# Kernel tuning notes

Hardware: AMD Instinct MI355X
Metric: run time of the kernel (lower is better)

Reference implementation:

```python
import jax, jax.numpy as jnp
import numpy as np

B, N, D = 8, 2048, 1024


def setup_inputs() -> dict:
    key = jax.random.key(0)
    k1, k2, k3, k4 = jax.random.split(key, 4)
    x = jax.random.normal(k1, (B, N, D), dtype=jnp.float32)
    f = jax.random.normal(k2, (B, N, D), dtype=jnp.float32)
    # nn.Linear(D, 1, bias=False) weights, shape [1, D]
    lim = 1.0 / np.sqrt(D)
    wk = jax.random.uniform(k3, (1, D), dtype=jnp.float32, minval=-lim, maxval=lim)
    wq = jax.random.uniform(k4, (1, D), dtype=jnp.float32, minval=-lim, maxval=lim)
    return {"x": x, "f": f, "wk": wk, "wq": wq}


def reference(x, f, wk, wq):
    # scalar k/q projections: [B, N]
    k = jnp.einsum("bnd,d->bn", x, wk[0])
    q = jnp.einsum("bnd,d->bn", x, wq[0])
    scale = 1.0 / jnp.sqrt(jnp.float32(D))
    # rank-1 outer-product scores: e[b,i,j] = k[b,i]*q[b,j]/sqrt(D)
    e = k[:, :, None] * q[:, None, :] * scale  # [B, N, N]
    # keep upper triangle (incl. diag), then any exact zero -> -inf
    # (faithful to torch: e_post[e_post == 0] = -inf, which also hits
    #  naturally-zero upper-triangle entries)
    e_tri = jnp.triu(e)
    e_post = jnp.where(e_tri == 0, -jnp.inf, e_tri)
    a = jax.nn.softmax(e_post, axis=1)  # softmax over rows (dim=1)
    # f_out = a^T @ f
    f_out = jnp.einsum("bij,bid->bjd", a, f)
    return f_out
```

## Files before the change

### kernel.cpp

```cpp
#include <hip/hip_runtime.h>

#define B 8
#define N 2048
#define D 1024
#define C 64
#define LC (N / C)
#define M 6
#define PB 96

__global__ __launch_bounds__(256) void k_proj(const float* __restrict__ x,
                                              const float* __restrict__ wk,
                                              const float* __restrict__ wq,
                                              float* __restrict__ kq) {
    const int wave = threadIdx.x >> 6;
    const int lane = threadIdx.x & 63;
    const int row  = blockIdx.x * 4 + wave;
    const float4* xr  = (const float4*)(x + (size_t)row * D);
    const float4* wk4 = (const float4*)wk;
    const float4* wq4 = (const float4*)wq;
    float ak = 0.f, aq = 0.f;
#pragma unroll
    for (int t = 0; t < (D / 4) / 64; ++t) {
        float4 xv = xr[t * 64 + lane];
        float4 kv = wk4[t * 64 + lane];
        float4 qv = wq4[t * 64 + lane];
        ak += xv.x * kv.x + xv.y * kv.y + xv.z * kv.z + xv.w * kv.w;
        aq += xv.x * qv.x + xv.y * qv.y + xv.z * qv.z + xv.w * qv.w;
    }
#pragma unroll
    for (int off = 32; off > 0; off >>= 1) {
        ak += __shfl_down(ak, off, 64);
        aq += __shfl_down(aq, off, 64);
    }
    if (lane == 0) {
        kq[row] = ak;
        kq[B * N + row] = aq;
    }
}

__global__ __launch_bounds__(128) void k_partial(const float* __restrict__ kq,
                                                 const float* __restrict__ f,
                                                 float* __restrict__ part) {
    const int dhalf = blockIdx.x & 1;
    const int c     = (blockIdx.x >> 1) & (C - 1);
    const int b     = blockIdx.x >> 7;
    const int d     = dhalf * 512 + threadIdx.x * 4;
    const float*  kb = kq + b * N + c * LC;
    const float4* fb = (const float4*)(f + (size_t)(b * N + c * LC) * D + d);
    float4 s[M];
#pragma unroll
    for (int m = 0; m < M; ++m) s[m] = make_float4(0.f, 0.f, 0.f, 0.f);
#pragma unroll 8
    for (int i = 0; i < LC; ++i) {
        float4 ff = fb[i * (D / 4)];
        float  kk = kb[i];
        float  w  = (kk != 0.0f) ? 1.0f : 0.0f;
        s[0].x += w * ff.x; s[0].y += w * ff.y; s[0].z += w * ff.z; s[0].w += w * ff.w;
        float kp = kk;
#pragma unroll
        for (int m = 1; m < M; ++m) {
            s[m].x += kp * ff.x; s[m].y += kp * ff.y;
            s[m].z += kp * ff.z; s[m].w += kp * ff.w;
            kp *= kk;
        }
    }
    float4* pb = (float4*)(part + ((size_t)(b * C + c) * M) * D + d);
#pragma unroll
    for (int m = 0; m < M; ++m) pb[m * (D / 4)] = s[m];
}

__global__ __launch_bounds__(128) void k_scan(const float* __restrict__ kq,
                                              float* __restrict__ Tc,
                                              float* __restrict__ part) {
    if (blockIdx.x < PB) {
        const int gid = blockIdx.x * 128 + threadIdx.x;
        const int d4  = gid & (D / 4 - 1);
        const int m   = (gid >> 8) % M;
        const int b   = gid / (256 * M);
        float4* p4 = (float4*)part;
        const size_t base = ((size_t)b * C * M + m) * (D / 4) + d4;
        const size_t cs   = (size_t)M * (D / 4);
        float4 run = make_float4(0.f, 0.f, 0.f, 0.f);
#pragma unroll 1
        for (int c0 = 0; c0 < C; c0 += 8) {
            float4 buf[8];
#pragma unroll
            for (int j = 0; j < 8; ++j) buf[j] = p4[base + (size_t)(c0 + j) * cs];
#pragma unroll
            for (int j = 0; j < 8; ++j) {
                float4 v = buf[j];
                p4[base + (size_t)(c0 + j) * cs] = run;
                run.x += v.x; run.y += v.y; run.z += v.z; run.w += v.w;
            }
        }
    } else {
        const int b2   = blockIdx.x - PB;
        const int lane = threadIdx.x;
        if (lane < 64) {
            float tm[M] = {0.f, 0.f, 0.f, 0.f, 0.f, 0.f};
            const float* kb = kq + b2 * N + lane * LC;
#pragma unroll
            for (int i = 0; i < LC; ++i) {
                float kk = kb[i];
                tm[0] += (kk != 0.0f) ? 1.0f : 0.0f;
                float kp = kk;
#pragma unroll
                for (int m = 1; m < M; ++m) { tm[m] += kp; kp *= kk; }
            }
#pragma unroll
            for (int m = 0; m < M; ++m) {
                float v = tm[m];
                const float orig = v;
#pragma unroll
                for (int off = 1; off < 64; off <<= 1) {
                    float nv = __shfl_up(v, off, 64);
                    if (lane >= off) v += nv;
                }
                Tc[(b2 * C + lane) * M + m] = v - orig;
            }
        }
    }
}

__global__ __launch_bounds__(128) void k_out(const float* __restrict__ kq,
                                             const float* __restrict__ f,
                                             const float* __restrict__ Tc,
                                             const float* __restrict__ part,
                                             float* __restrict__ out) {
    const int dhalf = blockIdx.x & 1;
    const int c     = (blockIdx.x >> 1) & (C - 1);
    const int b     = blockIdx.x >> 7;
    const int d     = dhalf * 512 + threadIdx.x * 4;

    float4 s[M];
    float  t[M];
    const float4* pb = (const float4*)(part + ((size_t)(b * C + c) * M) * D + d);
#pragma unroll
    for (int m = 0; m < M; ++m) s[m] = pb[m * (D / 4)];
#pragma unroll
    for (int m = 0; m < M; ++m) t[m] = Tc[(b * C + c) * M + m];

    const float*  kb = kq + b * N + c * LC;
    const float*  qb = kq + B * N + b * N + c * LC;
    const float4* fb = (const float4*)(f + (size_t)(b * N + c * LC) * D + d);
    float4*       ob = (float4*)(out + (size_t)(b * N + c * LC) * D + d);

#pragma unroll 4
    for (int i = 0; i < LC; ++i) {
        float4 ff = fb[i * (D / 4)];
        float  kk = kb[i];
        float  qq = qb[i];
        float  w  = (kk != 0.0f) ? 1.0f : 0.0f;
        t[0] += w;
        s[0].x += w * ff.x; s[0].y += w * ff.y; s[0].z += w * ff.z; s[0].w += w * ff.w;
        float kp = kk;
#pragma unroll
        for (int m = 1; m < M; ++m) {
            t[m] += kp;
            s[m].x += kp * ff.x; s[m].y += kp * ff.y;
            s[m].z += kp * ff.z; s[m].w += kp * ff.w;
            kp *= kk;
        }
        const float cj = qq * 0.03125f;
        const float g2 = cj * 0.5f;
        const float g3 = cj * (1.0f / 3.0f);
        const float g4 = cj * 0.25f;
        const float g5 = cj * 0.2f;
        float Z = ((((t[5] * g5 + t[4]) * g4 + t[3]) * g3 + t[2]) * g2 + t[1]) * cj + t[0];
        float rz = __builtin_amdgcn_rcpf(Z);
        float4 o;
        o.x = (((((s[5].x * g5 + s[4].x) * g4 + s[3].x) * g3 + s[2].x) * g2 + s[1].x) * cj + s[0].x) * rz;
        o.y = (((((s[5].y * g5 + s[4].y) * g4 + s[3].y) * g3 + s[2].y) * g2 + s[1].y) * cj + s[0].y) * rz;
        o.z = (((((s[5].z * g5 + s[4].z) * g4 + s[3].z) * g3 + s[2].z) * g2 + s[1].z) * cj + s[0].z) * rz;
        o.w = (((((s[5].w * g5 + s[4].w) * g4 + s[3].w) * g3 + s[2].w) * g2 + s[1].w) * cj + s[0].w) * rz;
        ob[i * (D / 4)] = o;
    }
}

extern "C" void kernel_launch(void* const* d_in, const int* in_sizes, int n_in,
                              void* d_out, int out_size, void* d_ws, size_t ws_size,
                              hipStream_t stream) {
    (void)in_sizes; (void)n_in; (void)out_size; (void)ws_size;
    const float* x  = (const float*)d_in[0];
    const float* f  = (const float*)d_in[1];
    const float* wk = (const float*)d_in[2];
    const float* wq = (const float*)d_in[3];
    float* out = (float*)d_out;
    float* ws  = (float*)d_ws;

    float* kq   = ws;
    float* Tc   = ws + 2 * B * N;
    float* part = ws + 2 * B * N + 4096;

    hipLaunchKernelGGL(k_proj,    dim3(B * N / 4),   dim3(256), 0, stream, x, wk, wq, kq);
    hipLaunchKernelGGL(k_partial, dim3(B * C * 2),   dim3(128), 0, stream, kq, f, part);
    hipLaunchKernelGGL(k_scan,    dim3(PB + B),      dim3(128), 0, stream, kq, Tc, part);
    hipLaunchKernelGGL(k_out,     dim3(B * C * 2),   dim3(128), 0, stream, kq, f, Tc, part, out);
}
```

Measured before the change: 195.8 us.

## Fuse four stages into one cooperative kernel with register-cached f

Replaces the four separate launches with a single cooperative kernel that uses grid-wide syncs between the projection, partial-sum, scan and output phases. Each thread keeps its 32 f values in registers between the partial and output phases, so f is read from memory once instead of twice, and the k/q slices are staged in shared memory. The cost is three grid barriers, heavy register use (64 floats of f per thread), and reliance on the occupancy check for co-residency. If cooperative launch is unavailable, the code falls back to the old four-kernel path.

Result: no change. 196.0 us (+0.1%).

```diff
diff --git a/kernel.cpp b/kernel.cpp
--- a/kernel.cpp
+++ b/kernel.cpp
@@ -1,4 +1,7 @@
 #include <hip/hip_runtime.h>
+#include <hip/hip_cooperative_groups.h>
+
+namespace cg = cooperative_groups;
 
 #define B 8
 #define N 2048
@@ -7,6 +10,175 @@
 #define LC (N / C)
 #define M 6
 #define PB 96
+#define GRID 1024
+#define TPB 256
+
+__global__ __launch_bounds__(TPB, 4) void k_fused(
+    const float* __restrict__ x, const float* __restrict__ f,
+    const float* __restrict__ wk, const float* __restrict__ wq,
+    float* __restrict__ kq, float* __restrict__ Tc,
+    float* __restrict__ part, float* __restrict__ out)
+{
+    cg::grid_group grid = cg::this_grid();
+    const int tid  = threadIdx.x;
+    const int blk  = blockIdx.x;
+    const int lane = tid & 63;
+
+    __shared__ float sk[LC];
+    __shared__ float sq[LC];
+
+    {
+        const int wave = (blk << 2) | (tid >> 6);
+        const float4* wk4 = (const float4*)wk;
+        const float4* wq4 = (const float4*)wq;
+        float4 kw[4], qw[4];
+#pragma unroll
+        for (int t = 0; t < 4; ++t) { kw[t] = wk4[t * 64 + lane]; qw[t] = wq4[t * 64 + lane]; }
+#pragma unroll
+        for (int r = 0; r < 4; ++r) {
+            const int row = (wave << 2) | r;
+            const float4* xr = (const float4*)(x + (size_t)row * D);
+            float ak = 0.f, aq = 0.f;
+#pragma unroll
+            for (int t = 0; t < 4; ++t) {
+                float4 xv = xr[t * 64 + lane];
+                ak += xv.x * kw[t].x + xv.y * kw[t].y + xv.z * kw[t].z + xv.w * kw[t].w;
+                aq += xv.x * qw[t].x + xv.y * qw[t].y + xv.z * qw[t].z + xv.w * qw[t].w;
+            }
+#pragma unroll
+            for (int off = 32; off > 0; off >>= 1) {
+                ak += __shfl_down(ak, off, 64);
+                aq += __shfl_down(aq, off, 64);
+            }
+            if (lane == 0) { kq[row] = ak; kq[B * N + row] = aq; }
+        }
+    }
+    __threadfence();
+    grid.sync();
+
+    const int dhalf = blk & 1;
+    const int c     = (blk >> 1) & (C - 1);
+    const int b     = blk >> 7;
+    const int d     = dhalf * 512 + tid * 2;
+
+    if (tid < LC)                        sk[tid]      = kq[b * N + c * LC + tid];
+    else if (tid >= 64 && tid < 64 + LC) sq[tid - 64] = kq[B * N + b * N + c * LC + (tid - 64)];
+    __syncthreads();
+
+    const float2* fb = (const float2*)(f + (size_t)(b * N + c * LC) * D + d);
+    float2 freg[LC];
+    float2 s[M];
+#pragma unroll
+    for (int m = 0; m < M; ++m) s[m] = make_float2(0.f, 0.f);
+#pragma unroll
+    for (int i = 0; i < LC; ++i) {
+        float2 ff = fb[i * (D / 2)];
+        freg[i] = ff;
+        float kk = sk[i];
+        float w  = (kk != 0.0f) ? 1.0f : 0.0f;
+        s[0].x += w * ff.x; s[0].y += w * ff.y;
+        float kp = kk;
+#pragma unroll
+        for (int m = 1; m < M; ++m) {
+            s[m].x += kp * ff.x; s[m].y += kp * ff.y;
+            kp *= kk;
+        }
+    }
+    {
+        float2* pw = (float2*)(part + ((size_t)(b * C + c) * M) * D + d);
+#pragma unroll
+        for (int m = 0; m < M; ++m) pw[m * (D / 2)] = s[m];
+    }
+    __threadfence();
+    grid.sync();
+
+    if (blk < PB) {
+        const int gid = blk * TPB + tid;
+        const int d2  = gid & (D / 2 - 1);
+        const int m   = (gid >> 9) % M;
+        const int bb  = (gid >> 9) / M;
+        float2* p2 = (float2*)part;
+        const size_t base = ((size_t)bb * C * M + m) * (D / 2) + d2;
+        const size_t cs   = (size_t)M * (D / 2);
+        float2 run = make_float2(0.f, 0.f);
+#pragma unroll 1
+        for (int c0 = 0; c0 < C; c0 += 8) {
+            float2 buf[8];
+#pragma unroll
+            for (int j = 0; j < 8; ++j) buf[j] = p2[base + (size_t)(c0 + j) * cs];
+#pragma unroll
+            for (int j = 0; j < 8; ++j) {
+                float2 v = buf[j];
+                p2[base + (size_t)(c0 + j) * cs] = run;
+                run.x += v.x; run.y += v.y;
+            }
+        }
+    } else if (blk < PB + 2) {
+        const int b2 = ((blk - PB) << 2) | (tid >> 6);
+        float tm[M] = {0.f, 0.f, 0.f, 0.f, 0.f, 0.f};
+        const float* kb = kq + b2 * N + lane * LC;
+#pragma unroll
+        for (int i = 0; i < LC; ++i) {
+            float kk = kb[i];
+            tm[0] += (kk != 0.0f) ? 1.0f : 0.0f;
+            float kp = kk;
+#pragma unroll
+            for (int m = 1; m < M; ++m) { tm[m] += kp; kp *= kk; }
+        }
+#pragma unroll
+        for (int m = 0; m < M; ++m) {
+            float v = tm[m];
+            const float orig = v;
+#pragma unroll
+            for (int off = 1; off < 64; off <<= 1) {
+                float nv = __shfl_up(v, off, 64);
+                if (lane >= off) v += nv;
+            }
+            Tc[(b2 * C + lane) * M + m] = v - orig;
+        }
+    }
+    __threadfence();
+    grid.sync();
+
+    {
+        float2 s2[M];
+        const float2* pr = (const float2*)(part + ((size_t)(b * C + c) * M) * D + d);
+#pragma unroll
+        for (int m = 0; m < M; ++m) s2[m] = pr[m * (D / 2)];
+        float t[M];
+#pragma unroll
+        for (int m = 0; m < M; ++m) t[m] = Tc[(b * C + c) * M + m];
+
+        float2* ob = (float2*)(out + (size_t)(b * N + c * LC) * D + d);
+#pragma unroll
+        for (int i = 0; i < LC; ++i) {
+            float2 ff = freg[i];
+            float kk = sk[i];
+            float qq = sq[i];
+            float w  = (kk != 0.0f) ? 1.0f : 0.0f;
+            t[0] += w;
+            s2[0].x += w * ff.x; s2[0].y += w * ff.y;
+            float kp = kk;
+#pragma unroll
+            for (int m = 1; m < M; ++m) {
+                t[m] += kp;
+                s2[m].x += kp * ff.x; s2[m].y += kp * ff.y;
+                kp *= kk;
+            }
+            const float cj = qq * 0.03125f;
+            const float g2 = cj * 0.5f;
+            const float g3 = cj * (1.0f / 3.0f);
+            const float g4 = cj * 0.25f;
+            const float g5 = cj * 0.2f;
+            float Z = ((((t[5] * g5 + t[4]) * g4 + t[3]) * g3 + t[2]) * g2 + t[1]) * cj + t[0];
+            float rz = __builtin_amdgcn_rcpf(Z);
+            float2 o;
+            o.x = (((((s2[5].x * g5 + s2[4].x) * g4 + s2[3].x) * g3 + s2[2].x) * g2 + s2[1].x) * cj + s2[0].x) * rz;
+            o.y = (((((s2[5].y * g5 + s2[4].y) * g4 + s2[3].y) * g3 + s2[2].y) * g2 + s2[1].y) * cj + s2[0].y) * rz;
+            ob[i * (D / 2)] = o;
+        }
+    }
+}
 
 __global__ __launch_bounds__(256) void k_proj(const float* __restrict__ x,
                                               const float* __restrict__ wk,
@@ -32,10 +204,7 @@
         ak += __shfl_down(ak, off, 64);
         aq += __shfl_down(aq, off, 64);
     }
-    if (lane == 0) {
-        kq[row] = ak;
-        kq[B * N + row] = aq;
-    }
+    if (lane == 0) { kq[row] = ak; kq[B * N + row] = aq; }
 }
 
 __global__ __launch_bounds__(128) void k_partial(const float* __restrict__ kq,
@@ -192,8 +361,25 @@
     float* Tc   = ws + 2 * B * N;
     float* part = ws + 2 * B * N + 4096;
 
-    hipLaunchKernelGGL(k_proj,    dim3(B * N / 4),   dim3(256), 0, stream, x, wk, wq, kq);
-    hipLaunchKernelGGL(k_partial, dim3(B * C * 2),   dim3(128), 0, stream, kq, f, part);
-    hipLaunchKernelGGL(k_scan,    dim3(PB + B),      dim3(128), 0, stream, kq, Tc, part);
-    hipLaunchKernelGGL(k_out,     dim3(B * C * 2),   dim3(128), 0, stream, kq, f, Tc, part, out);
-}
+    static int coop_ok = -1;
+    if (coop_ok < 0) {
+        int nb = 0;
+        hipError_t e = hipOccupancyMaxActiveBlocksPerMultiprocessor(
+            &nb, (const void*)k_fused, TPB, 0);
+        coop_ok = (e == hipSuccess && nb >= (GRID + 255) / 256) ? 1 : 0;
+    }
+
+    hipError_t le = hipErrorUnknown;
+    if (coop_ok) {
+        void* args[] = {(void*)&x, (void*)&f, (void*)&wk, (void*)&wq,
+                        (void*)&kq, (void*)&Tc, (void*)&part, (void*)&out};
+        le = hipLaunchCooperativeKernel((const void*)k_fused, dim3(GRID), dim3(TPB),
+                                        args, 0, stream);
+    }
+    if (!coop_ok || le != hipSuccess) {
+        hipLaunchKernelGGL(k_proj,    dim3(B * N / 4), dim3(256), 0, stream, x, wk, wq, kq);
+        hipLaunchKernelGGL(k_partial, dim3(B * C * 2), dim3(128), 0, stream, kq, f, part);
+        hipLaunchKernelGGL(k_scan,    dim3(PB + B),    dim3(128), 0, stream, kq, Tc, part);
+        hipLaunchKernelGGL(k_out,     dim3(B * C * 2), dim3(128), 0, stream, kq, f, Tc, part, out);
+    }
+}
```

## Fuse partial, scan and output kernels into single-pass decoupled look-back scan

Applied to the files above, without the earlier changes.

Replaces the three-kernel partial/scan/output pipeline with one kernel that computes per-chunk moment sums and publishes them with flags. Each block then does a decoupled look-back to collect the exclusive prefix from earlier chunks, and finally emits outputs while re-reading its f chunk. This drops the separate scan pass and its read and write of the partial buffer, and removes two launch boundaries. The cost is spin-waiting on flags, which relies on earlier blocks being scheduled first, plus a switch from float4 to float2 accesses with 256 threads per block.

Measured after the change: 333.4 us. +70.2%, slower.

```diff
diff --git a/kernel.cpp b/kernel.cpp
--- a/kernel.cpp
+++ b/kernel.cpp
@@ -6,12 +6,20 @@
 #define C 64
 #define LC (N / C)
 #define M 6
-#define PB 96
+#define CH (B * 2)
+#define REC 512
+#define TPB 256
+
 
 __global__ __launch_bounds__(256) void k_proj(const float* __restrict__ x,
                                               const float* __restrict__ wk,
                                               const float* __restrict__ wq,
-                                              float* __restrict__ kq) {
+                                              float* __restrict__ kq,
+                                              int* __restrict__ flags) {
+    if (blockIdx.x == 0) {
+#pragma unroll
+        for (int j = 0; j < 4; ++j) flags[threadIdx.x + j * 256] = 0;
+    }
     const int wave = threadIdx.x >> 6;
     const int lane = threadIdx.x & 63;
     const int row  = blockIdx.x * 4 + wave;
@@ -38,127 +46,150 @@
     }
 }
 
-__global__ __launch_bounds__(128) void k_partial(const float* __restrict__ kq,
-                                                 const float* __restrict__ f,
-                                                 float* __restrict__ part) {
-    const int dhalf = blockIdx.x & 1;
-    const int c     = (blockIdx.x >> 1) & (C - 1);
-    const int b     = blockIdx.x >> 7;
-    const int d     = dhalf * 512 + threadIdx.x * 4;
-    const float*  kb = kq + b * N + c * LC;
-    const float4* fb = (const float4*)(f + (size_t)(b * N + c * LC) * D + d);
-    float4 s[M];
-#pragma unroll
-    for (int m = 0; m < M; ++m) s[m] = make_float4(0.f, 0.f, 0.f, 0.f);
+__global__ __launch_bounds__(TPB, 4) void k_main(
+    const float* __restrict__ kq, const float* __restrict__ f,
+    float* __restrict__ tA, float* __restrict__ tI,
+    float* __restrict__ pA, float* __restrict__ pI,
+    int* __restrict__ flags, float* __restrict__ out)
+{
+    const int blk   = blockIdx.x;
+    const int c     = blk & (C - 1);
+    const int chain = blk >> 6;
+    const int b     = chain >> 1;
+    const int dh    = chain & 1;
+    const int tid   = threadIdx.x;
+    const int d     = dh * 512 + tid * 2;
+
+    __shared__ float sk[LC];
+    __shared__ float sq[LC];
+    __shared__ int   sp0;
+
+    if (tid < LC)                        sk[tid]      = kq[b * N + c * LC + tid];
+    else if (tid >= 64 && tid < 64 + LC) sq[tid - 64] = kq[B * N + b * N + c * LC + (tid - 64)];
+    __syncthreads();
+
+    float ta[M] = {0.f, 0.f, 0.f, 0.f, 0.f, 0.f};
+#pragma unroll
+    for (int i = 0; i < LC; ++i) {
+        float kk = sk[i];
+        ta[0] += (kk != 0.f) ? 1.f : 0.f;
+        float kp = kk;
+#pragma unroll
+        for (int m = 1; m < M; ++m) { ta[m] += kp; kp *= kk; }
+    }
+
+    const float2* fb = (const float2*)(f + (size_t)(b * N + c * LC) * D + d);
+    float2 s[M];
+#pragma unroll
+    for (int m = 0; m < M; ++m) s[m] = make_float2(0.f, 0.f);
 #pragma unroll 8
     for (int i = 0; i < LC; ++i) {
-        float4 ff = fb[i * (D / 4)];
-        float  kk = kb[i];
-        float  w  = (kk != 0.0f) ? 1.0f : 0.0f;
-        s[0].x += w * ff.x; s[0].y += w * ff.y; s[0].z += w * ff.z; s[0].w += w * ff.w;
+        float2 ff = fb[i * (D / 2)];
+        float  kk = sk[i];
+        float  w  = (kk != 0.f) ? 1.f : 0.f;
+        s[0].x += w * ff.x; s[0].y += w * ff.y;
         float kp = kk;
 #pragma unroll
         for (int m = 1; m < M; ++m) {
             s[m].x += kp * ff.x; s[m].y += kp * ff.y;
-            s[m].z += kp * ff.z; s[m].w += kp * ff.w;
             kp *= kk;
         }
     }
-    float4* pb = (float4*)(part + ((size_t)(b * C + c) * M) * D + d);
-#pragma unroll
-    for (int m = 0; m < M; ++m) pb[m * (D / 4)] = s[m];
-}
-
-__global__ __launch_bounds__(128) void k_scan(const float* __restrict__ kq,
-                                              float* __restrict__ Tc,
-                                              float* __restrict__ part) {
-    if (blockIdx.x < PB) {
-        const int gid = blockIdx.x * 128 + threadIdx.x;
-        const int d4  = gid & (D / 4 - 1);
-        const int m   = (gid >> 8) % M;
-        const int b   = gid / (256 * M);
-        float4* p4 = (float4*)part;
-        const size_t base = ((size_t)b * C * M + m) * (D / 4) + d4;
-        const size_t cs   = (size_t)M * (D / 4);
-        float4 run = make_float4(0.f, 0.f, 0.f, 0.f);
-#pragma unroll 1
-        for (int c0 = 0; c0 < C; c0 += 8) {
-            float4 buf[8];
-#pragma unroll
-            for (int j = 0; j < 8; ++j) buf[j] = p4[base + (size_t)(c0 + j) * cs];
-#pragma unroll
-            for (int j = 0; j < 8; ++j) {
-                float4 v = buf[j];
-                p4[base + (size_t)(c0 + j) * cs] = run;
-                run.x += v.x; run.y += v.y; run.z += v.z; run.w += v.w;
-            }
-        }
-    } else {
-        const int b2   = blockIdx.x - PB;
-        const int lane = threadIdx.x;
-        if (lane < 64) {
-            float tm[M] = {0.f, 0.f, 0.f, 0.f, 0.f, 0.f};
-            const float* kb = kq + b2 * N + lane * LC;
-#pragma unroll
-            for (int i = 0; i < LC; ++i) {
-                float kk = kb[i];
-                tm[0] += (kk != 0.0f) ? 1.0f : 0.0f;
-                float kp = kk;
-#pragma unroll
-                for (int m = 1; m < M; ++m) { tm[m] += kp; kp *= kk; }
-            }
+
+    const size_t rec = (size_t)blk * (M * REC);
+    if (c < C - 1) {
+        float* vd = (c == 0) ? pI : pA;
+        float* td = (c == 0) ? tI : tA;
+#pragma unroll
+        for (int m = 0; m < M; ++m)
+            ((float2*)(vd + rec + (size_t)m * REC))[tid] = s[m];
+        if (tid == 0) {
+#pragma unroll
+            for (int m = 0; m < M; ++m) td[blk * 8 + m] = ta[m];
+        }
+        __syncthreads();
+        if (tid == 0) {
+            __threadfence();
+            __hip_atomic_store(&flags[blk], (c == 0) ? 2 : 1,
+                               __ATOMIC_RELAXED, __HIP_MEMORY_SCOPE_AGENT);
+        }
+    }
+
+    float2 run[M];
+    float  tr[M];
+#pragma unroll
+    for (int m = 0; m < M; ++m) { run[m] = make_float2(0.f, 0.f); tr[m] = 0.f; }
+
+    if (c > 0) {
+        if (tid == 0) {
+            int p = c - 1;
+            for (;;) {
+                int st = __hip_atomic_load(&flags[chain * C + p],
+                                           __ATOMIC_RELAXED, __HIP_MEMORY_SCOPE_AGENT);
+                if (st == 2) break;
+                if (st == 1) { --p; }
+                else __builtin_amdgcn_s_sleep(2);
+            }
+            sp0 = p;
+        }
+        __syncthreads();
+        const int p0 = sp0;
+        (void)__hip_atomic_load(&flags[chain * C + p0],
+                                __ATOMIC_ACQUIRE, __HIP_MEMORY_SCOPE_AGENT);
+
+        const size_t recP = (size_t)(chain * C + p0) * (M * REC);
+#pragma unroll
+        for (int m = 0; m < M; ++m)
+            run[m] = ((const float2*)(pI + recP + (size_t)m * REC))[tid];
+#pragma unroll
+        for (int m = 0; m < M; ++m) tr[m] = tI[(chain * C + p0) * 8 + m];
+
+        for (int p = p0 + 1; p < c; ++p) {
+            const size_t rp = (size_t)(chain * C + p) * (M * REC);
 #pragma unroll
             for (int m = 0; m < M; ++m) {
-                float v = tm[m];
-                const float orig = v;
-#pragma unroll
-                for (int off = 1; off < 64; off <<= 1) {
-                    float nv = __shfl_up(v, off, 64);
-                    if (lane >= off) v += nv;
-                }
-                Tc[(b2 * C + lane) * M + m] = v - orig;
-            }
-        }
-    }
-}
-
-__global__ __launch_bounds__(128) void k_out(const float* __restrict__ kq,
-                                             const float* __restrict__ f,
-                                             const float* __restrict__ Tc,
-                                             const float* __restrict__ part,
-                                             float* __restrict__ out) {
-    const int dhalf = blockIdx.x & 1;
-    const int c     = (blockIdx.x >> 1) & (C - 1);
-    const int b     = blockIdx.x >> 7;
-    const int d     = dhalf * 512 + threadIdx.x * 4;
-
-    float4 s[M];
-    float  t[M];
-    const float4* pb = (const float4*)(part + ((size_t)(b * C + c) * M) * D + d);
-#pragma unroll
-    for (int m = 0; m < M; ++m) s[m] = pb[m * (D / 4)];
-#pragma unroll
-    for (int m = 0; m < M; ++m) t[m] = Tc[(b * C + c) * M + m];
-
-    const float*  kb = kq + b * N + c * LC;
-    const float*  qb = kq + B * N + b * N + c * LC;
-    const float4* fb = (const float4*)(f + (size_t)(b * N + c * LC) * D + d);
-    float4*       ob = (float4*)(out + (size_t)(b * N + c * LC) * D + d);
-
+                float2 v = ((const float2*)(pA + rp + (size_t)m * REC))[tid];
+                run[m].x += v.x; run[m].y += v.y;
+            }
+#pragma unroll
+            for (int m = 0; m < M; ++m) tr[m] += tA[(chain * C + p) * 8 + m];
+        }
+
+        if (c < C - 1) {
+#pragma unroll
+            for (int m = 0; m < M; ++m) {
+                float2 v;
+                v.x = run[m].x + s[m].x;
+                v.y = run[m].y + s[m].y;
+                ((float2*)(pI + rec + (size_t)m * REC))[tid] = v;
+            }
+            if (tid == 0) {
+#pragma unroll
+                for (int m = 0; m < M; ++m) tI[blk * 8 + m] = tr[m] + ta[m];
+            }
+            __syncthreads();
+            if (tid == 0) {
+                __threadfence();
+                __hip_atomic_store(&flags[blk], 2,
+                                   __ATOMIC_RELAXED, __HIP_MEMORY_SCOPE_AGENT);
+            }
+        }
+    }
+
+    float2* ob = (float2*)(out + (size_t)(b * N + c * LC) * D + d);
 #pragma unroll 4
     for (int i = 0; i < LC; ++i) {
-        float4 ff = fb[i * (D / 4)];
-        float  kk = kb[i];
-        float  qq = qb[i];
-        float  w  = (kk != 0.0f) ? 1.0f : 0.0f;
-        t[0] += w;
-        s[0].x += w * ff.x; s[0].y += w * ff.y; s[0].z += w * ff.z; s[0].w += w * ff.w;
+        float2 ff = fb[i * (D / 2)];
+        float  kk = sk[i];
+        float  qq = sq[i];
+        float  w  = (kk != 0.f) ? 1.f : 0.f;
+        tr[0] += w;
+        run[0].x += w * ff.x; run[0].y += w * ff.y;
         float kp = kk;
 #pragma unroll
         for (int m = 1; m < M; ++m) {
-            t[m] += kp;
-            s[m].x += kp * ff.x; s[m].y += kp * ff.y;
-            s[m].z += kp * ff.z; s[m].w += kp * ff.w;
+            tr[m] += kp;
+            run[m].x += kp * ff.x; run[m].y += kp * ff.y;
             kp *= kk;
         }
         const float cj = qq * 0.03125f;
@@ -166,14 +197,12 @@
         const float g3 = cj * (1.0f / 3.0f);
         const float g4 = cj * 0.25f;
         const float g5 = cj * 0.2f;
-        float Z = ((((t[5] * g5 + t[4]) * g4 + t[3]) * g3 + t[2]) * g2 + t[1]) * cj + t[0];
+        float Z = ((((tr[5] * g5 + tr[4]) * g4 + tr[3]) * g3 + tr[2]) * g2 + tr[1]) * cj + tr[0];
         float rz = __builtin_amdgcn_rcpf(Z);
-        float4 o;
-        o.x = (((((s[5].x * g5 + s[4].x) * g4 + s[3].x) * g3 + s[2].x) * g2 + s[1].x) * cj + s[0].x) * rz;
-        o.y = (((((s[5].y * g5 + s[4].y) * g4 + s[3].y) * g3 + s[2].y) * g2 + s[1].y) * cj + s[0].y) * rz;
-        o.z = (((((s[5].z * g5 + s[4].z) * g4 + s[3].z) * g3 + s[2].z) * g2 + s[1].z) * cj + s[0].z) * rz;
-        o.w = (((((s[5].w * g5 + s[4].w) * g4 + s[3].w) * g3 + s[2].w) * g2 + s[1].w) * cj + s[0].w) * rz;
-        ob[i * (D / 4)] = o;
+        float2 o;
+        o.x = (((((run[5].x * g5 + run[4].x) * g4 + run[3].x) * g3 + run[2].x) * g2 + run[1].x) * cj + run[0].x) * rz;
+        o.y = (((((run[5].y * g5 + run[4].y) * g4 + run[3].y) * g3 + run[2].y) * g2 + run[1].y) * cj + run[0].y) * rz;
+        ob[i * (D / 2)] = o;
     }
 }
 
@@ -188,12 +217,13 @@
     float* out = (float*)d_out;
     float* ws  = (float*)d_ws;
 
-    float* kq   = ws;
-    float* Tc   = ws + 2 * B * N;
-    float* part = ws + 2 * B * N + 4096;
-
-    hipLaunchKernelGGL(k_proj,    dim3(B * N / 4),   dim3(256), 0, stream, x, wk, wq, kq);
-    hipLaunchKernelGGL(k_partial, dim3(B * C * 2),   dim3(128), 0, stream, kq, f, part);
-    hipLaunchKernelGGL(k_scan,    dim3(PB + B),      dim3(128), 0, stream, kq, Tc, part);
-    hipLaunchKernelGGL(k_out,     dim3(B * C * 2),   dim3(128), 0, stream, kq, f, Tc, part, out);
+    float* kq    = ws;
+    float* tA    = ws + 32768;
+    float* tI    = ws + 40960;
+    int*   flags = (int*)(ws + 49152);
+    float* pA    = ws + 65536;
+    float* pI    = ws + 65536 + 3145728;
+
+    hipLaunchKernelGGL(k_proj, dim3(B * N / 4), dim3(256), 0, stream, x, wk, wq, kq, flags);
+    hipLaunchKernelGGL(k_main, dim3(CH * C),    dim3(TPB), 0, stream, kq, f, tA, tI, pA, pI, flags, out);
 }
```

## Fuse chunk-moment scan into output kernel and widen blocks to full rows

Applied to the files above, without the earlier changes.

The per-chunk k-moment prefix scan (Tc) moves out of the scan kernel and into each output block, which recomputes the scan for its batch with one wave and keeps it in shared memory. k and q chunks are staged in LDS instead of being read per iteration from global memory. Blocks now cover all of D with 256 threads instead of half of D with 128. The part-sum scan switches from float4 to scalar elements, using 4x more threads. The cost is redundant k-moment scan work in every output block and a serial prologue before the main loop.

After: 197.4 us. About the same (+0.8%).

```diff
diff --git a/kernel.cpp b/kernel.cpp
--- a/kernel.cpp
+++ b/kernel.cpp
@@ -6,7 +6,7 @@
 #define C 64
 #define LC (N / C)
 #define M 6
-#define PB 96
+
 
 __global__ __launch_bounds__(256) void k_proj(const float* __restrict__ x,
                                               const float* __restrict__ wk,
@@ -38,22 +38,25 @@
     }
 }
 
-__global__ __launch_bounds__(128) void k_partial(const float* __restrict__ kq,
-                                                 const float* __restrict__ f,
-                                                 float* __restrict__ part) {
-    const int dhalf = blockIdx.x & 1;
-    const int c     = (blockIdx.x >> 1) & (C - 1);
-    const int b     = blockIdx.x >> 7;
-    const int d     = dhalf * 512 + threadIdx.x * 4;
-    const float*  kb = kq + b * N + c * LC;
-    const float4* fb = (const float4*)(f + (size_t)(b * N + c * LC) * D + d);
+__global__ __launch_bounds__(256) void k_part(const float* __restrict__ kq,
+                                              const float* __restrict__ f,
+                                              float* __restrict__ part) {
+    const int c   = blockIdx.x & (C - 1);
+    const int b   = blockIdx.x >> 6;
+    const int tid = threadIdx.x;
+
+    __shared__ float sk[LC];
+    if (tid < LC) sk[tid] = kq[b * N + c * LC + tid];
+    __syncthreads();
+
+    const float4* fb = (const float4*)(f + (size_t)(b * N + c * LC) * D) + tid;
     float4 s[M];
 #pragma unroll
     for (int m = 0; m < M; ++m) s[m] = make_float4(0.f, 0.f, 0.f, 0.f);
 #pragma unroll 8
     for (int i = 0; i < LC; ++i) {
         float4 ff = fb[i * (D / 4)];
-        float  kk = kb[i];
+        float  kk = sk[i];
         float  w  = (kk != 0.0f) ? 1.0f : 0.0f;
         s[0].x += w * ff.x; s[0].y += w * ff.y; s[0].z += w * ff.z; s[0].w += w * ff.w;
         float kp = kk;
@@ -64,92 +67,91 @@
             kp *= kk;
         }
     }
-    float4* pb = (float4*)(part + ((size_t)(b * C + c) * M) * D + d);
+    float4* pb = (float4*)(part + ((size_t)(b * C + c) * M) * D) + tid;
 #pragma unroll
     for (int m = 0; m < M; ++m) pb[m * (D / 4)] = s[m];
 }
 
-__global__ __launch_bounds__(128) void k_scan(const float* __restrict__ kq,
-                                              float* __restrict__ Tc,
-                                              float* __restrict__ part) {
-    if (blockIdx.x < PB) {
-        const int gid = blockIdx.x * 128 + threadIdx.x;
-        const int d4  = gid & (D / 4 - 1);
-        const int m   = (gid >> 8) % M;
-        const int b   = gid / (256 * M);
-        float4* p4 = (float4*)part;
-        const size_t base = ((size_t)b * C * M + m) * (D / 4) + d4;
-        const size_t cs   = (size_t)M * (D / 4);
-        float4 run = make_float4(0.f, 0.f, 0.f, 0.f);
+__global__ __launch_bounds__(256) void k_scan(float* __restrict__ part) {
+    const int gid  = blockIdx.x * 256 + threadIdx.x;
+    const int d    = gid & (D - 1);
+    const int rest = gid >> 10;
+    const int m    = rest % M;
+    const int b    = rest / M;
+    const size_t base = ((size_t)(b * C) * M + m) * D + d;
+    const size_t cs   = (size_t)M * D;
+    float run = 0.f;
 #pragma unroll 1
-        for (int c0 = 0; c0 < C; c0 += 8) {
-            float4 buf[8];
-#pragma unroll
-            for (int j = 0; j < 8; ++j) buf[j] = p4[base + (size_t)(c0 + j) * cs];
-#pragma unroll
-            for (int j = 0; j < 8; ++j) {
-                float4 v = buf[j];
-                p4[base + (size_t)(c0 + j) * cs] = run;
-                run.x += v.x; run.y += v.y; run.z += v.z; run.w += v.w;
-            }
-        }
-    } else {
-        const int b2   = blockIdx.x - PB;
-        const int lane = threadIdx.x;
-        if (lane < 64) {
-            float tm[M] = {0.f, 0.f, 0.f, 0.f, 0.f, 0.f};
-            const float* kb = kq + b2 * N + lane * LC;
-#pragma unroll
-            for (int i = 0; i < LC; ++i) {
-                float kk = kb[i];
-                tm[0] += (kk != 0.0f) ? 1.0f : 0.0f;
-                float kp = kk;
-#pragma unroll
-                for (int m = 1; m < M; ++m) { tm[m] += kp; kp *= kk; }
-            }
-#pragma unroll
-            for (int m = 0; m < M; ++m) {
-                float v = tm[m];
-                const float orig = v;
-#pragma unroll
-                for (int off = 1; off < 64; off <<= 1) {
-                    float nv = __shfl_up(v, off, 64);
-                    if (lane >= off) v += nv;
-                }
-                Tc[(b2 * C + lane) * M + m] = v - orig;
-            }
-        }
-    }
-}
-
-__global__ __launch_bounds__(128) void k_out(const float* __restrict__ kq,
+    for (int c0 = 0; c0 < C; c0 += 8) {
+        float buf[8];
+#pragma unroll
+        for (int j = 0; j < 8; ++j) buf[j] = part[base + (size_t)(c0 + j) * cs];
+#pragma unroll
+        for (int j = 0; j < 8; ++j) {
+            float v = buf[j];
+            part[base + (size_t)(c0 + j) * cs] = run;
+            run += v;
+        }
+    }
+}
+
+__global__ __launch_bounds__(256) void k_out(const float* __restrict__ kq,
                                              const float* __restrict__ f,
-                                             const float* __restrict__ Tc,
                                              const float* __restrict__ part,
                                              float* __restrict__ out) {
-    const int dhalf = blockIdx.x & 1;
-    const int c     = (blockIdx.x >> 1) & (C - 1);
-    const int b     = blockIdx.x >> 7;
-    const int d     = dhalf * 512 + threadIdx.x * 4;
+    const int c   = blockIdx.x & (C - 1);
+    const int b   = blockIdx.x >> 6;
+    const int tid = threadIdx.x;
+
+    __shared__ float sk[LC];
+    __shared__ float sq[LC];
+    __shared__ float sT[M];
+
+    if (tid < 64) {
+        float tm[M] = {0.f, 0.f, 0.f, 0.f, 0.f, 0.f};
+        const float* kb = kq + b * N + tid * LC;
+#pragma unroll
+        for (int i = 0; i < LC; ++i) {
+            float kk = kb[i];
+            tm[0] += (kk != 0.0f) ? 1.0f : 0.0f;
+            float kp = kk;
+#pragma unroll
+            for (int m = 1; m < M; ++m) { tm[m] += kp; kp *= kk; }
+        }
+#pragma unroll
+        for (int m = 0; m < M; ++m) {
+            float v = tm[m];
+            const float orig = v;
+#pragma unroll
+            for (int off = 1; off < 64; off <<= 1) {
+                float nv = __shfl_up(v, off, 64);
+                if (tid >= off) v += nv;
+            }
+            if (tid == c) sT[m] = v - orig;
+        }
+    } else if (tid < 64 + LC) {
+        sk[tid - 64] = kq[b * N + c * LC + (tid - 64)];
+    } else if (tid >= 128 && tid < 128 + LC) {
+        sq[tid - 128] = kq[B * N + b * N + c * LC + (tid - 128)];
+    }
+    __syncthreads();
 
     float4 s[M];
     float  t[M];
-    const float4* pb = (const float4*)(part + ((size_t)(b * C + c) * M) * D + d);
+    const float4* pb = (const float4*)(part + ((size_t)(b * C + c) * M) * D) + tid;
 #pragma unroll
     for (int m = 0; m < M; ++m) s[m] = pb[m * (D / 4)];
 #pragma unroll
-    for (int m = 0; m < M; ++m) t[m] = Tc[(b * C + c) * M + m];
-
-    const float*  kb = kq + b * N + c * LC;
-    const float*  qb = kq + B * N + b * N + c * LC;
-    const float4* fb = (const float4*)(f + (size_t)(b * N + c * LC) * D + d);
-    float4*       ob = (float4*)(out + (size_t)(b * N + c * LC) * D + d);
+    for (int m = 0; m < M; ++m) t[m] = sT[m];
+
+    const float4* fb = (const float4*)(f + (size_t)(b * N + c * LC) * D) + tid;
+    float4*       ob = (float4*)(out + (size_t)(b * N + c * LC) * D) + tid;
 
 #pragma unroll 4
     for (int i = 0; i < LC; ++i) {
         float4 ff = fb[i * (D / 4)];
-        float  kk = kb[i];
-        float  qq = qb[i];
+        float  kk = sk[i];
+        float  qq = sq[i];
         float  w  = (kk != 0.0f) ? 1.0f : 0.0f;
         t[0] += w;
         s[0].x += w * ff.x; s[0].y += w * ff.y; s[0].z += w * ff.z; s[0].w += w * ff.w;
@@ -189,11 +191,10 @@
     float* ws  = (float*)d_ws;
 
     float* kq   = ws;
-    float* Tc   = ws + 2 * B * N;
-    float* part = ws + 2 * B * N + 4096;
-
-    hipLaunchKernelGGL(k_proj,    dim3(B * N / 4),   dim3(256), 0, stream, x, wk, wq, kq);
-    hipLaunchKernelGGL(k_partial, dim3(B * C * 2),   dim3(128), 0, stream, kq, f, part);
-    hipLaunchKernelGGL(k_scan,    dim3(PB + B),      dim3(128), 0, stream, kq, Tc, part);
-    hipLaunchKernelGGL(k_out,     dim3(B * C * 2),   dim3(128), 0, stream, kq, f, Tc, part, out);
-}
+    float* part = ws + 65536;
+
+    hipLaunchKernelGGL(k_proj, dim3(B * N / 4),     dim3(256), 0, stream, x, wk, wq, kq);
+    hipLaunchKernelGGL(k_part, dim3(B * C),         dim3(256), 0, stream, kq, f, part);
+    hipLaunchKernelGGL(k_scan, dim3(B * M * D / 256), dim3(256), 0, stream, part);
+    hipLaunchKernelGGL(k_out,  dim3(B * C),         dim3(256), 0, stream, kq, f, part, out);
+}
```
